# Kernel tuning notes

Hardware: AMD Instinct MI355X
Metric: run time of the kernel (lower is better)

Reference implementation:

```python
import jax, jax.numpy as jnp
import numpy as np

B, S, D_MODEL, NUM_HEADS, DFF = 4, 2048, 256, 8, 1024
DEPTH = D_MODEL // NUM_HEADS
EPS = 1e-6
LENGTH_SCALE = 1.0


def setup_inputs() -> dict:
    key = jax.random.key(0)
    ks = jax.random.split(key, 18)
    n = lambda k, shp, s=0.05: (jax.random.normal(k, shp, dtype=jnp.float32) * s)
    return {
        "x": jax.random.normal(ks[0], (B, S, D_MODEL), dtype=jnp.float32),
        "wq_w": n(ks[1], (D_MODEL, D_MODEL)), "wq_b": jnp.zeros((D_MODEL,), jnp.float32),
        "wk_w": n(ks[2], (D_MODEL, D_MODEL)), "wk_b": jnp.zeros((D_MODEL,), jnp.float32),
        "wv_w": n(ks[3], (D_MODEL, D_MODEL)), "wv_b": jnp.zeros((D_MODEL,), jnp.float32),
        "wo_w": n(ks[4], (D_MODEL, D_MODEL)), "wo_b": jnp.zeros((D_MODEL,), jnp.float32),
        "ffn1_w": n(ks[5], (D_MODEL, DFF)), "ffn1_b": jnp.zeros((DFF,), jnp.float32),
        "ffn2_w": n(ks[6], (DFF, D_MODEL)), "ffn2_b": jnp.zeros((D_MODEL,), jnp.float32),
        "ln1_g": jnp.ones((D_MODEL,), jnp.float32), "ln1_b": jnp.zeros((D_MODEL,), jnp.float32),
        "ln2_g": jnp.ones((D_MODEL,), jnp.float32), "ln2_b": jnp.zeros((D_MODEL,), jnp.float32),
    }


def _layernorm(x, g, b):
    mu = jnp.mean(x, axis=-1, keepdims=True)
    var = jnp.mean(jnp.square(x - mu), axis=-1, keepdims=True)
    return (x - mu) * jax.lax.rsqrt(var + EPS) * g + b


def _split_heads(t):
    # [B,S,D_MODEL] -> [B,H,S,depth]
    return t.reshape(B, S, NUM_HEADS, DEPTH).transpose(0, 2, 1, 3)


def _encoder_layer(x, wq_w, wq_b, wk_w, wk_b, wv_w, wv_b, wo_w, wo_b,
                   ffn1_w, ffn1_b, ffn2_w, ffn2_b, ln1_g, ln1_b, ln2_g, ln2_b):
    q = _split_heads(x @ wq_w + wq_b)
    k = _split_heads(x @ wk_w + wk_b)
    v = _split_heads(x @ wv_w + wv_b)
    # pairwise squared distances: ||q||^2 - 2 q.k + ||k||^2 -> [B,H,S,S]
    q2 = jnp.sum(q * q, axis=-1)  # [B,H,S]
    k2 = jnp.sum(k * k, axis=-1)  # [B,H,S]
    dists = q2[..., :, None] - 2.0 * jnp.einsum("bhqd,bhkd->bhqk", q, k) + k2[..., None, :]
    # exponentiated-quadratic kernel, then softmax over keys (mask=None)
    attn = jax.nn.softmax(jnp.exp(-0.5 * dists / (LENGTH_SCALE ** 2)), axis=-1)
    out = jnp.einsum("bhqk,bhkd->bhqd", attn, v)  # [B,H,S,depth]
    out = out.transpose(0, 2, 1, 3).reshape(B, S, D_MODEL)
    attn_out = out @ wo_w + wo_b
    # dropout is identity (training=False)
    out1 = _layernorm(x + attn_out, ln1_g, ln1_b)
    ffn = jax.nn.relu(out1 @ ffn1_w + ffn1_b) @ ffn2_w + ffn2_b
    return _layernorm(out1 + ffn, ln2_g, ln2_b)


def reference(x, wq_w, wq_b, wk_w, wk_b, wv_w, wv_b, wo_w, wo_b,
              ffn1_w, ffn1_b, ffn2_w, ffn2_b, ln1_g, ln1_b, ln2_g, ln2_b):
    return _encoder_layer(x, wq_w, wq_b, wk_w, wk_b, wv_w, wv_b, wo_w, wo_b,
                          ffn1_w, ffn1_b, ffn2_w, ffn2_b, ln1_g, ln1_b, ln2_g, ln2_b)
```

## Files before the change

kernel.cpp:

```cpp
#include <hip/hip_runtime.h>
#include <hip/hip_bf16.h>

#define SQL  2048
#define DM   256
#define LNEPS 1e-6f
#define NLOG2E_H (-0.72134752f)
#define LOG2E    (1.44269504f)

#define B_XB    (0ull)
#define B_QB    (4ull<<20)
#define B_KB    (8ull<<20)
#define B_VB    (12ull<<20)
#define B_CTX   (16ull<<20)
#define B_O1B   (20ull<<20)
#define B_MID   (24ull<<20)
#define B_WQKVT (40ull<<20)
#define B_WOT   (41ull<<20)
#define B_W1T   (42ull<<20)
#define B_W2T   (43ull<<20)
#define B_BQKV  (44ull<<20)
#define B_HQ    (45ull<<20)
#define B_HK    (46ull<<20)
#define B_C1    (47ull<<20)
#define B_O1F   (55ull<<20)
#define B_C2    (63ull<<20)

typedef float  f32x16 __attribute__((ext_vector_type(16)));
typedef short  bf16x8 __attribute__((ext_vector_type(8)));
typedef int    i32x4  __attribute__((ext_vector_type(4)));
typedef int    i32x2  __attribute__((ext_vector_type(2)));

static __device__ __forceinline__ unsigned short bfu(float f){
    __hip_bfloat16 h = __float2bfloat16(f);
    return *reinterpret_cast<unsigned short*>(&h);
}
static __device__ __forceinline__ unsigned pk2(float a, float b){
    return (unsigned)bfu(a) | ((unsigned)bfu(b) << 16);
}
static __device__ __forceinline__ void glds16(const void* g, void* l){
    __builtin_amdgcn_global_load_lds((const __attribute__((address_space(1))) unsigned int*)g,
                                     (__attribute__((address_space(3))) unsigned int*)l, 16, 0, 0);
}

__global__ __launch_bounds__(256) void k_pack(const float* __restrict__ W,
                                              unsigned short* __restrict__ Wt,
                                              int K, int N)
{
    __shared__ float tile[32][33];
    const int t = threadIdx.x;
    const int tx = t & 31, ty = t >> 5;
    const int kb = blockIdx.x * 32, nb = blockIdx.y * 32;
#pragma unroll
    for (int i = 0; i < 32; i += 8) tile[ty + i][tx] = W[(size_t)(kb + ty + i) * N + nb + tx];
    __syncthreads();
#pragma unroll
    for (int i = 0; i < 32; i += 8) Wt[(size_t)(nb + ty + i) * K + kb + tx] = bfu(tile[tx][ty + i]);
}

__global__ __launch_bounds__(256) void k_packb(const float* __restrict__ bq,
                                               const float* __restrict__ bk,
                                               const float* __restrict__ bv,
                                               float* __restrict__ bqkv)
{
    const int wb = blockIdx.x;
    const float* s = (wb == 0) ? bq : (wb == 1 ? bk : bv);
    bqkv[wb * 256 + threadIdx.x] = s[threadIdx.x];
}

__global__ __launch_bounds__(256) void k_xb(const float* __restrict__ x,
                                            unsigned short* __restrict__ xb)
{
    const int i = blockIdx.x * 256 + threadIdx.x;
    float4 v = ((const float4*)x)[i];
    ushort4 o; o.x = bfu(v.x); o.y = bfu(v.y); o.z = bfu(v.z); o.w = bfu(v.w);
    ((ushort4*)xb)[i] = o;
}

__global__ __launch_bounds__(256, 2) void k_qkv(
    const unsigned short* __restrict__ A, const unsigned short* __restrict__ Bt,
    const float* __restrict__ bias,
    unsigned short* __restrict__ qb, unsigned short* __restrict__ kb,
    unsigned short* __restrict__ vb)
{
    __shared__ __align__(16) char As[16384];
    __shared__ __align__(16) char Bs[16384];
    const int t = threadIdx.x;
    const int lane = t & 63, w = t >> 6;
    const int lo = lane & 31, hi = lane >> 5;
    const int row0 = blockIdx.x * 128;
    const int col0 = blockIdx.y * 128;
    f32x16 acc[2][2] = {};
    const int gS = lane & 7;

    for (int kt = 0; kt < 4; ++kt) {
        const int k0 = kt * 64;
#pragma unroll
        for (int i = 0; i < 4; ++i) {
            const int r = w * 32 + i * 8 + (lane >> 3);
            glds16((const char*)(A  + (size_t)(row0 + r) * 256 + k0) + ((gS ^ (r & 7)) << 4),
                   As + w * 4096 + i * 1024 + lane * 16);
            glds16((const char*)(Bt + (size_t)(col0 + r) * 256 + k0) + ((gS ^ (r & 7)) << 4),
                   Bs + w * 4096 + i * 1024 + lane * 16);
        }
        __syncthreads();
        const int rA = (w >> 1) * 64 + lo;
        const int rB = (w & 1) * 64 + lo;
#pragma unroll
        for (int s = 0; s < 4; ++s) {
            const int g = s * 2 + hi;
            bf16x8 fa0 = *(const bf16x8*)(As + rA * 128 + ((g ^ (rA & 7)) << 4));
            bf16x8 fa1 = *(const bf16x8*)(As + (rA + 32) * 128 + ((g ^ (rA & 7)) << 4));
            bf16x8 fb0 = *(const bf16x8*)(Bs + rB * 128 + ((g ^ (rB & 7)) << 4));
            bf16x8 fb1 = *(const bf16x8*)(Bs + (rB + 32) * 128 + ((g ^ (rB & 7)) << 4));
            acc[0][0] = __builtin_amdgcn_mfma_f32_32x32x16_bf16(fa0, fb0, acc[0][0], 0, 0, 0);
            acc[0][1] = __builtin_amdgcn_mfma_f32_32x32x16_bf16(fa0, fb1, acc[0][1], 0, 0, 0);
            acc[1][0] = __builtin_amdgcn_mfma_f32_32x32x16_bf16(fa1, fb0, acc[1][0], 0, 0, 0);
            acc[1][1] = __builtin_amdgcn_mfma_f32_32x32x16_bf16(fa1, fb1, acc[1][1], 0, 0, 0);
        }
        __syncthreads();
    }
#pragma unroll
    for (int m = 0; m < 2; ++m)
#pragma unroll
    for (int n = 0; n < 2; ++n) {
        const int c0 = col0 + (w & 1) * 64 + n * 32;
        const int which = c0 >> 8, h = (c0 >> 5) & 7;
        unsigned short* dst = (which == 0) ? qb : (which == 1 ? kb : vb);
        const float bv = bias[c0 + lo];
#pragma unroll
        for (int r = 0; r < 16; ++r) {
            const int gr = row0 + (w >> 1) * 64 + m * 32 + (r & 3) + 8 * (r >> 2) + 4 * hi;
            const int b = gr >> 11, s = gr & 2047;
            dst[(((size_t)(b * 8 + h)) * SQL + s) * 32 + lo] = bfu(acc[m][n][r] + bv);
        }
    }
}

__global__ __launch_bounds__(256) void k_h2(const unsigned short* __restrict__ qb,
                                            const unsigned short* __restrict__ kb,
                                            float* __restrict__ hq, float* __restrict__ hk)
{
    const int gid = blockIdx.x * 256 + threadIdx.x;
    const unsigned short* qp = qb + (size_t)gid * 32;
    const unsigned short* kp = kb + (size_t)gid * 32;
    float sq = 0.f, sk = 0.f;
#pragma unroll
    for (int i = 0; i < 4; ++i) {
        i32x4 qv = *(const i32x4*)(qp + i * 8);
        i32x4 kv = *(const i32x4*)(kp + i * 8);
#pragma unroll
        for (int j = 0; j < 4; ++j) {
            unsigned int qw = (unsigned int)qv[j], kw = (unsigned int)kv[j];
            float a = __builtin_bit_cast(float, qw << 16);
            float c = __builtin_bit_cast(float, qw & 0xffff0000u);
            float d = __builtin_bit_cast(float, kw << 16);
            float e = __builtin_bit_cast(float, kw & 0xffff0000u);
            sq += a * a + c * c; sk += d * d + e * e;
        }
    }
    hq[gid] = NLOG2E_H * sq;
    hk[gid] = NLOG2E_H * sk;
}

__global__ __launch_bounds__(256) void k_attn(
    const unsigned short* __restrict__ qg, const unsigned short* __restrict__ kg,
    const unsigned short* __restrict__ vg, const float* __restrict__ hq,
    const float* __restrict__ hk, unsigned short* __restrict__ ctxb)
{
    __shared__ __align__(16) char kls[4096];
    __shared__ __align__(16) char vtl[4096];
    __shared__ __align__(16) float hks[64];
    __shared__ __align__(16) float invs[128];

    const int t = threadIdx.x;
    const int lane = t & 63;
    const int wv_ = t >> 6;
    const int lo = lane & 31;
    const int hi = lane >> 5;

    const int bid = blockIdx.x;
    const int qchunk = bid & 15;
    const int bh = bid >> 4;
    const int b = bh >> 3, h = bh & 7;

    const int qrow = qchunk * 128 + wv_ * 32 + lo;
    const unsigned short* qp = qg + ((size_t)bh * SQL + qrow) * 32;
    bf16x8 qf[2];
    qf[0] = *(const bf16x8*)(qp + hi * 8);
    qf[1] = *(const bf16x8*)(qp + 16 + hi * 8);
    const float hqv = hq[(size_t)bh * SQL + qrow];

    f32x16 acc = {};
    float den = 0.f;

    const int vr_key = t >> 2;
    const int vr_g   = t & 3;
    const unsigned short* kbg = kg + (size_t)bh * SQL * 32;
    const unsigned short* vbg = vg + (size_t)bh * SQL * 32;

    for (int kt = 0; kt < 32; ++kt) {
        const int key0 = kt * 64;
        {
            const int r = (wv_ << 4) + (lane >> 2);
            const int gl = lane & 3;
            glds16((const char*)(kbg + (size_t)(key0 + r) * 32) + ((gl ^ ((r >> 1) & 3)) << 4),
                   kls + wv_ * 1024 + lane * 16);
            const unsigned short* vr = vbg + (size_t)(key0 + vr_key) * 32 + vr_g * 8;
            i32x4 vl = *(const i32x4*)vr;
#pragma unroll
            for (int j2 = 0; j2 < 4; ++j2) {
                unsigned int wrd = (unsigned int)vl[j2];
                const int d0 = vr_g * 8 + j2 * 2;
                *(unsigned short*)(vtl + d0 * 128 + ((vr_key * 2) ^ ((d0 & 7) << 4))) = (unsigned short)(wrd & 0xffff);
                *(unsigned short*)(vtl + (d0 + 1) * 128 + ((vr_key * 2) ^ (((d0 + 1) & 7) << 4))) = (unsigned short)(wrd >> 16);
            }
            if (t < 64) hks[t] = hk[(size_t)bh * SQL + key0 + t];
        }
        __syncthreads();

#pragma unroll
        for (int h2 = 0; h2 < 2; ++h2) {
            const int kb32 = h2 * 32;
            const int kA = kb32 + lo;
            const char* krow = kls + kA * 64;
            const int ksw = (kA >> 1) & 3;
            bf16x8 kf0 = *(const bf16x8*)(krow + (((0 + hi) ^ ksw) << 4));
            bf16x8 kf1 = *(const bf16x8*)(krow + (((2 + hi) ^ ksw) << 4));
            f32x16 sc = {};
            sc = __builtin_amdgcn_mfma_f32_32x32x16_bf16(kf0, qf[0], sc, 0, 0, 0);
            sc = __builtin_amdgcn_mfma_f32_32x32x16_bf16(kf1, qf[1], sc, 0, 0, 0);
            float4 h0 = *(const float4*)&hks[kb32 + 4 * hi];
            float4 h1 = *(const float4*)&hks[kb32 + 8 + 4 * hi];
            float4 h2v = *(const float4*)&hks[kb32 + 16 + 4 * hi];
            float4 h3 = *(const float4*)&hks[kb32 + 24 + 4 * hi];
            float hkv[16] = {h0.x,h0.y,h0.z,h0.w, h1.x,h1.y,h1.z,h1.w,
                             h2v.x,h2v.y,h2v.z,h2v.w, h3.x,h3.y,h3.z,h3.w};
            float w[16];
#pragma unroll
            for (int r = 0; r < 16; ++r) {
                float arg = fmaf(sc[r], LOG2E, hqv + hkv[r]);
                float e1  = __builtin_amdgcn_exp2f(arg);
                float ww  = __builtin_amdgcn_exp2f(e1 * LOG2E);
                den += ww;
                w[r] = ww;
            }
            i32x4 p0; p0[0]=pk2(w[0],w[1]);  p0[1]=pk2(w[2],w[3]);
                      p0[2]=pk2(w[4],w[5]);  p0[3]=pk2(w[6],w[7]);
            i32x4 p1; p1[0]=pk2(w[8],w[9]);  p1[1]=pk2(w[10],w[11]);
                      p1[2]=pk2(w[12],w[13]); p1[3]=pk2(w[14],w[15]);
            const char* vrow = vtl + lo * 128;
            const int vxor = (lo & 7) << 4;
            const int o0 = (kb32 + 4 * hi) * 2;
            const int o1 = (kb32 + 16 + 4 * hi) * 2;
            i32x2 a0 = *(const i32x2*)(vrow + (o0 ^ vxor));
            i32x2 a1 = *(const i32x2*)(vrow + ((o0 + 16) ^ vxor));
            i32x2 b0 = *(const i32x2*)(vrow + (o1 ^ vxor));
            i32x2 b1 = *(const i32x2*)(vrow + ((o1 + 16) ^ vxor));
            i32x4 vb0; vb0[0]=a0[0]; vb0[1]=a0[1]; vb0[2]=a1[0]; vb0[3]=a1[1];
            i32x4 vb1; vb1[0]=b0[0]; vb1[1]=b0[1]; vb1[2]=b1[0]; vb1[3]=b1[1];
            acc = __builtin_amdgcn_mfma_f32_32x32x16_bf16(
                __builtin_bit_cast(bf16x8, p0), __builtin_bit_cast(bf16x8, vb0), acc, 0, 0, 0);
            acc = __builtin_amdgcn_mfma_f32_32x32x16_bf16(
                __builtin_bit_cast(bf16x8, p1), __builtin_bit_cast(bf16x8, vb1), acc, 0, 0, 0);
        }
        __syncthreads();
    }

    const float dfull = den + __shfl_xor(den, 32);
    if (lane < 32) invs[wv_ * 32 + lo] = 1.f / dfull;
    __syncthreads();
    float4 i0 = *(const float4*)&invs[wv_ * 32 + 4 * hi];
    float4 i1 = *(const float4*)&invs[wv_ * 32 + 8 + 4 * hi];
    float4 i2 = *(const float4*)&invs[wv_ * 32 + 16 + 4 * hi];
    float4 i3 = *(const float4*)&invs[wv_ * 32 + 24 + 4 * hi];
    float iv[16] = {i0.x,i0.y,i0.z,i0.w, i1.x,i1.y,i1.z,i1.w,
                    i2.x,i2.y,i2.z,i2.w, i3.x,i3.y,i3.z,i3.w};
    unsigned short* cbase = ctxb + ((size_t)(b * SQL + qchunk * 128 + wv_ * 32)) * 256 + h * 32 + lo;
#pragma unroll
    for (int r = 0; r < 16; ++r) {
        const int qr = (r & 3) + 8 * (r >> 2) + 4 * hi;
        cbase[(size_t)qr * 256] = bfu(acc[r] * iv[r]);
    }
}

template<int KDIM, int NFULL, int RELU, int RESID, int OUTF, int OUTB>
__global__ __launch_bounds__(256, 2) void k_gemm(
    const unsigned short* __restrict__ A, const unsigned short* __restrict__ Bt,
    const float* __restrict__ bias, const float* __restrict__ resid,
    float* __restrict__ outf, unsigned short* __restrict__ outb)
{
    __shared__ __align__(16) char As[16384];
    __shared__ __align__(16) char Bs[16384];
    const int t = threadIdx.x;
    const int lane = t & 63, w = t >> 6;
    const int lo = lane & 31, hi = lane >> 5;
    const int row0 = blockIdx.x * 128;
    const int col0 = blockIdx.y * 128;
    f32x16 acc[2][2] = {};
    const int gS = lane & 7;

    for (int kt = 0; kt < KDIM / 64; ++kt) {
        const int k0 = kt * 64;
#pragma unroll
        for (int i = 0; i < 4; ++i) {
            const int r = w * 32 + i * 8 + (lane >> 3);
            glds16((const char*)(A  + (size_t)(row0 + r) * KDIM + k0) + ((gS ^ (r & 7)) << 4),
                   As + w * 4096 + i * 1024 + lane * 16);
            glds16((const char*)(Bt + (size_t)(col0 + r) * KDIM + k0) + ((gS ^ (r & 7)) << 4),
                   Bs + w * 4096 + i * 1024 + lane * 16);
        }
        __syncthreads();
        const int rA = (w >> 1) * 64 + lo;
        const int rB = (w & 1) * 64 + lo;
#pragma unroll
        for (int s = 0; s < 4; ++s) {
            const int g = s * 2 + hi;
            bf16x8 fa0 = *(const bf16x8*)(As + rA * 128 + ((g ^ (rA & 7)) << 4));
            bf16x8 fa1 = *(const bf16x8*)(As + (rA + 32) * 128 + ((g ^ (rA & 7)) << 4));
            bf16x8 fb0 = *(const bf16x8*)(Bs + rB * 128 + ((g ^ (rB & 7)) << 4));
            bf16x8 fb1 = *(const bf16x8*)(Bs + (rB + 32) * 128 + ((g ^ (rB & 7)) << 4));
            acc[0][0] = __builtin_amdgcn_mfma_f32_32x32x16_bf16(fa0, fb0, acc[0][0], 0, 0, 0);
            acc[0][1] = __builtin_amdgcn_mfma_f32_32x32x16_bf16(fa0, fb1, acc[0][1], 0, 0, 0);
            acc[1][0] = __builtin_amdgcn_mfma_f32_32x32x16_bf16(fa1, fb0, acc[1][0], 0, 0, 0);
            acc[1][1] = __builtin_amdgcn_mfma_f32_32x32x16_bf16(fa1, fb1, acc[1][1], 0, 0, 0);
        }
        __syncthreads();
    }
#pragma unroll
    for (int m = 0; m < 2; ++m)
#pragma unroll
    for (int n = 0; n < 2; ++n) {
        const int c0 = col0 + (w & 1) * 64 + n * 32;
        const float bv = bias[c0 + lo];
#pragma unroll
        for (int r = 0; r < 16; ++r) {
            const int gr = row0 + (w >> 1) * 64 + m * 32 + (r & 3) + 8 * (r >> 2) + 4 * hi;
            float vv = acc[m][n][r] + bv;
            if (RESID) vv += resid[(size_t)gr * NFULL + c0 + lo];
            if (RELU)  vv = fmaxf(vv, 0.f);
            if (OUTF)  outf[(size_t)gr * NFULL + c0 + lo] = vv;
            if (OUTB)  outb[(size_t)gr * NFULL + c0 + lo] = bfu(vv);
        }
    }
}

template<int DUAL>
__global__ __launch_bounds__(256) void k_ln(const float* __restrict__ in,
                                            const float* __restrict__ g,
                                            const float* __restrict__ bt,
                                            float* __restrict__ outf,
                                            unsigned short* __restrict__ outb)
{
    const int row = blockIdx.x * 4 + (threadIdx.x >> 6);
    const int lane = threadIdx.x & 63;
    const float4 v = ((const float4*)(in + (size_t)row * 256))[lane];
    float s  = v.x + v.y + v.z + v.w;
    float ss = v.x * v.x + v.y * v.y + v.z * v.z + v.w * v.w;
#pragma unroll
    for (int off = 32; off; off >>= 1) { s += __shfl_xor(s, off); ss += __shfl_xor(ss, off); }
    const float mu = s * (1.f / 256.f);
    const float rstd = rsqrtf(ss * (1.f / 256.f) - mu * mu + LNEPS);
    const float4 gg = ((const float4*)g)[lane];
    const float4 bb = ((const float4*)bt)[lane];
    float4 o;
    o.x = (v.x - mu) * rstd * gg.x + bb.x;
    o.y = (v.y - mu) * rstd * gg.y + bb.y;
    o.z = (v.z - mu) * rstd * gg.z + bb.z;
    o.w = (v.w - mu) * rstd * gg.w + bb.w;
    ((float4*)(outf + (size_t)row * 256))[lane] = o;
    if (DUAL) {
        ushort4 ob; ob.x = bfu(o.x); ob.y = bfu(o.y); ob.z = bfu(o.z); ob.w = bfu(o.w);
        ((ushort4*)(outb + (size_t)row * 256))[lane] = ob;
    }
}

extern "C" void kernel_launch(void* const* d_in, const int* in_sizes, int n_in,
                              void* d_out, int out_size, void* d_ws, size_t ws_size,
                              hipStream_t stream) {
    const float* x   = (const float*)d_in[0];
    const float* wq  = (const float*)d_in[1];  const float* bq  = (const float*)d_in[2];
    const float* wk  = (const float*)d_in[3];  const float* bk  = (const float*)d_in[4];
    const float* wv  = (const float*)d_in[5];  const float* bv  = (const float*)d_in[6];
    const float* wo  = (const float*)d_in[7];  const float* wob = (const float*)d_in[8];
    const float* w1  = (const float*)d_in[9];  const float* b1  = (const float*)d_in[10];
    const float* w2  = (const float*)d_in[11]; const float* b2  = (const float*)d_in[12];
    const float* g1  = (const float*)d_in[13]; const float* bl1 = (const float*)d_in[14];
    const float* g2  = (const float*)d_in[15]; const float* bl2 = (const float*)d_in[16];

    char* ws = (char*)d_ws;
    unsigned short* xb    = (unsigned short*)(ws + B_XB);
    unsigned short* qb    = (unsigned short*)(ws + B_QB);
    unsigned short* kbuf  = (unsigned short*)(ws + B_KB);
    unsigned short* vbuf  = (unsigned short*)(ws + B_VB);
    unsigned short* ctxb  = (unsigned short*)(ws + B_CTX);
    unsigned short* o1b   = (unsigned short*)(ws + B_O1B);
    unsigned short* mid   = (unsigned short*)(ws + B_MID);
    unsigned short* wqkvT = (unsigned short*)(ws + B_WQKVT);
    unsigned short* woT   = (unsigned short*)(ws + B_WOT);
    unsigned short* w1T   = (unsigned short*)(ws + B_W1T);
    unsigned short* w2T   = (unsigned short*)(ws + B_W2T);
    float* bqkv = (float*)(ws + B_BQKV);
    float* hqb  = (float*)(ws + B_HQ);
    float* hkb  = (float*)(ws + B_HK);
    float* c1   = (float*)(ws + B_C1);
    float* o1f  = (float*)(ws + B_O1F);
    float* c2   = (float*)(ws + B_C2);
    float* out  = (float*)d_out;

    k_pack<<<dim3(8, 8),  dim3(256), 0, stream>>>(wq, wqkvT,             256, 256);
    k_pack<<<dim3(8, 8),  dim3(256), 0, stream>>>(wk, wqkvT + 256 * 256, 256, 256);
    k_pack<<<dim3(8, 8),  dim3(256), 0, stream>>>(wv, wqkvT + 512 * 256, 256, 256);
    k_pack<<<dim3(8, 8),  dim3(256), 0, stream>>>(wo, woT,               256, 256);
    k_pack<<<dim3(8, 32), dim3(256), 0, stream>>>(w1, w1T,               256, 1024);
    k_pack<<<dim3(32, 8), dim3(256), 0, stream>>>(w2, w2T,               1024, 256);
    k_packb<<<dim3(3), dim3(256), 0, stream>>>(bq, bk, bv, bqkv);
    k_xb<<<dim3(2048), dim3(256), 0, stream>>>(x, xb);

    k_qkv<<<dim3(64, 6), dim3(256), 0, stream>>>(xb, wqkvT, bqkv, qb, kbuf, vbuf);
    k_h2<<<dim3(256), dim3(256), 0, stream>>>(qb, kbuf, hqb, hkb);
    k_attn<<<dim3(512), dim3(256), 0, stream>>>(qb, kbuf, vbuf, hqb, hkb, ctxb);
    k_gemm<256, 256, 0, 1, 1, 0><<<dim3(64, 2), dim3(256), 0, stream>>>(ctxb, woT, wob, x, c1, nullptr);
    k_ln<1><<<dim3(2048), dim3(256), 0, stream>>>(c1, g1, bl1, o1f, o1b);

    k_gemm<256, 1024, 1, 0, 0, 1><<<dim3(64, 8), dim3(256), 0, stream>>>(o1b, w1T, b1, nullptr, nullptr, mid);
    k_gemm<1024, 256, 0, 1, 1, 0><<<dim3(64, 2), dim3(256), 0, stream>>>(mid, w2T, b2, o1f, c2, nullptr);
    k_ln<0><<<dim3(2048), dim3(256), 0, stream>>>(c2, g2, bl2, out, nullptr);
}
```

Baseline: 227.6 us.

## Split attention keys across two groups, pre-transpose V, split-K GEMMs, merge pack kernels

Folds the six weight-pack launches, the bias pack and the x conversion into one kernel. The QKV GEMM now writes V pre-transposed and swizzled, so attention can load it straight to LDS with global_load_lds instead of transposing it by hand. Attention runs 512-thread blocks where two groups each take half the keys and reduce through LDS at the end. The Wo and FFN2 GEMMs use split-K into two partial buffers, summed together with the residual inside the layernorm kernel. This raises parallelism and cuts launch count, at the cost of extra partial-sum traffic and an LDS reduction.

```diff
diff --git a/kernel.cpp b/kernel.cpp
--- a/kernel.cpp
+++ b/kernel.cpp
@@ -10,20 +10,19 @@
 #define B_XB    (0ull)
 #define B_QB    (4ull<<20)
 #define B_KB    (8ull<<20)
-#define B_VB    (12ull<<20)
+#define B_VT    (12ull<<20)
 #define B_CTX   (16ull<<20)
 #define B_O1B   (20ull<<20)
-#define B_MID   (24ull<<20)
-#define B_WQKVT (40ull<<20)
-#define B_WOT   (41ull<<20)
-#define B_W1T   (42ull<<20)
-#define B_W2T   (43ull<<20)
-#define B_BQKV  (44ull<<20)
-#define B_HQ    (45ull<<20)
-#define B_HK    (46ull<<20)
-#define B_C1    (47ull<<20)
-#define B_O1F   (55ull<<20)
-#define B_C2    (63ull<<20)
+#define B_O1F   (24ull<<20)
+#define B_MID   (32ull<<20)
+#define B_WQKVT (48ull<<20)
+#define B_WOT   ((48ull<<20)+(512ull<<10))
+#define B_W1T   (49ull<<20)
+#define B_W2T   ((49ull<<20)+(512ull<<10))
+#define B_BQKV  (50ull<<20)
+#define B_HQ    ((50ull<<20)+(64ull<<10))
+#define B_HK    ((50ull<<20)+(320ull<<10))
+#define B_C2    (0ull)
 
 typedef float  f32x16 __attribute__((ext_vector_type(16)));
 typedef short  bf16x8 __attribute__((ext_vector_type(8)));
@@ -42,45 +41,59 @@
                                      (__attribute__((address_space(3))) unsigned int*)l, 16, 0, 0);
 }
 
-__global__ __launch_bounds__(256) void k_pack(const float* __restrict__ W,
-                                              unsigned short* __restrict__ Wt,
-                                              int K, int N)
+__global__ __launch_bounds__(256) void k_packall(
+    const float* __restrict__ wq, const float* __restrict__ wk, const float* __restrict__ wv,
+    const float* __restrict__ wo, const float* __restrict__ w1, const float* __restrict__ w2,
+    const float* __restrict__ bq, const float* __restrict__ bk, const float* __restrict__ bv,
+    const float* __restrict__ x,
+    unsigned short* __restrict__ wqkvT, unsigned short* __restrict__ woT,
+    unsigned short* __restrict__ w1T, unsigned short* __restrict__ w2T,
+    float* __restrict__ bqkv, unsigned short* __restrict__ xb)
 {
     __shared__ float tile[32][33];
+    const int bid = blockIdx.x;
     const int t = threadIdx.x;
-    const int tx = t & 31, ty = t >> 5;
-    const int kb = blockIdx.x * 32, nb = blockIdx.y * 32;
-#pragma unroll
-    for (int i = 0; i < 32; i += 8) tile[ty + i][tx] = W[(size_t)(kb + ty + i) * N + nb + tx];
-    __syncthreads();
-#pragma unroll
-    for (int i = 0; i < 32; i += 8) Wt[(size_t)(nb + ty + i) * K + kb + tx] = bfu(tile[tx][ty + i]);
-}
-
-__global__ __launch_bounds__(256) void k_packb(const float* __restrict__ bq,
-                                               const float* __restrict__ bk,
-                                               const float* __restrict__ bv,
-                                               float* __restrict__ bqkv)
-{
-    const int wb = blockIdx.x;
-    const float* s = (wb == 0) ? bq : (wb == 1 ? bk : bv);
-    bqkv[wb * 256 + threadIdx.x] = s[threadIdx.x];
-}
-
-__global__ __launch_bounds__(256) void k_xb(const float* __restrict__ x,
-                                            unsigned short* __restrict__ xb)
-{
-    const int i = blockIdx.x * 256 + threadIdx.x;
-    float4 v = ((const float4*)x)[i];
-    ushort4 o; o.x = bfu(v.x); o.y = bfu(v.y); o.z = bfu(v.z); o.w = bfu(v.w);
-    ((ushort4*)xb)[i] = o;
+    if (bid < 768) {
+        const float* W; unsigned short* Wt; int K, N, xk, yn;
+        if (bid < 192) {
+            int which = bid >> 6, local = bid & 63;
+            W = (which == 0) ? wq : (which == 1 ? wk : wv);
+            Wt = wqkvT + which * 65536; K = 256; N = 256;
+            xk = local & 7; yn = local >> 3;
+        } else if (bid < 256) {
+            int local = bid - 192; W = wo; Wt = woT; K = 256; N = 256;
+            xk = local & 7; yn = local >> 3;
+        } else if (bid < 512) {
+            int local = bid - 256; W = w1; Wt = w1T; K = 256; N = 1024;
+            xk = local & 7; yn = local >> 3;
+        } else {
+            int local = bid - 512; W = w2; Wt = w2T; K = 1024; N = 256;
+            xk = local & 31; yn = local >> 5;
+        }
+        const int tx = t & 31, ty = t >> 5;
+        const int kb = xk * 32, nb = yn * 32;
+#pragma unroll
+        for (int i = 0; i < 32; i += 8) tile[ty + i][tx] = W[(size_t)(kb + ty + i) * N + nb + tx];
+        __syncthreads();
+#pragma unroll
+        for (int i = 0; i < 32; i += 8) Wt[(size_t)(nb + ty + i) * K + kb + tx] = bfu(tile[tx][ty + i]);
+    } else if (bid < 771) {
+        int wb = bid - 768;
+        const float* s = (wb == 0) ? bq : (wb == 1 ? bk : bv);
+        bqkv[wb * 256 + t] = s[t];
+    } else {
+        const int i = (bid - 771) * 256 + t;
+        float4 v = ((const float4*)x)[i];
+        ushort4 o; o.x = bfu(v.x); o.y = bfu(v.y); o.z = bfu(v.z); o.w = bfu(v.w);
+        ((ushort4*)xb)[i] = o;
+    }
 }
 
 __global__ __launch_bounds__(256, 2) void k_qkv(
     const unsigned short* __restrict__ A, const unsigned short* __restrict__ Bt,
     const float* __restrict__ bias,
     unsigned short* __restrict__ qb, unsigned short* __restrict__ kb,
-    unsigned short* __restrict__ vb)
+    char* __restrict__ vtg)
 {
     __shared__ __align__(16) char As[16384];
     __shared__ __align__(16) char Bs[16384];
@@ -125,13 +138,25 @@
     for (int n = 0; n < 2; ++n) {
         const int c0 = col0 + (w & 1) * 64 + n * 32;
         const int which = c0 >> 8, h = (c0 >> 5) & 7;
-        unsigned short* dst = (which == 0) ? qb : (which == 1 ? kb : vb);
         const float bv = bias[c0 + lo];
-#pragma unroll
-        for (int r = 0; r < 16; ++r) {
-            const int gr = row0 + (w >> 1) * 64 + m * 32 + (r & 3) + 8 * (r >> 2) + 4 * hi;
-            const int b = gr >> 11, s = gr & 2047;
-            dst[(((size_t)(b * 8 + h)) * SQL + s) * 32 + lo] = bfu(acc[m][n][r] + bv);
+        if (which < 2) {
+            unsigned short* dst = (which == 0) ? qb : kb;
+#pragma unroll
+            for (int r = 0; r < 16; ++r) {
+                const int gr = row0 + (w >> 1) * 64 + m * 32 + (r & 3) + 8 * (r >> 2) + 4 * hi;
+                const int b = gr >> 11, s = gr & 2047;
+                dst[(((size_t)(b * 8 + h)) * SQL + s) * 32 + lo] = bfu(acc[m][n][r] + bv);
+            }
+        } else {
+#pragma unroll
+            for (int r = 0; r < 16; ++r) {
+                const int gr = row0 + (w >> 1) * 64 + m * 32 + (r & 3) + 8 * (r >> 2) + 4 * hi;
+                const int b = gr >> 11, s = gr & 2047;
+                const int o = s * 2;
+                const int op = (o & ~0x78) | ((((o >> 3) & 15) ^ (lo & 15)) << 3);
+                *(unsigned short*)(vtg + ((size_t)(b * 8 + h)) * 131072 + (size_t)lo * 4096 + op)
+                    = bfu(acc[m][n][r] + bv);
+            }
         }
     }
 }
@@ -162,26 +187,29 @@
     hk[gid] = NLOG2E_H * sk;
 }
 
-__global__ __launch_bounds__(256) void k_attn(
+__global__ __launch_bounds__(512, 4) void k_attn(
     const unsigned short* __restrict__ qg, const unsigned short* __restrict__ kg,
-    const unsigned short* __restrict__ vg, const float* __restrict__ hq,
+    const char* __restrict__ vtg, const float* __restrict__ hq,
     const float* __restrict__ hk, unsigned short* __restrict__ ctxb)
 {
-    __shared__ __align__(16) char kls[4096];
-    __shared__ __align__(16) char vtl[4096];
-    __shared__ __align__(16) float hks[64];
+    __shared__ __align__(16) char kls[8192];
+    __shared__ __align__(16) char vtl[8192];
+    __shared__ __align__(16) float hks[128];
+    __shared__ __align__(16) float redacc[16 * 256];
+    __shared__ __align__(16) float redden[256];
     __shared__ __align__(16) float invs[128];
 
     const int t = threadIdx.x;
+    const int grp = t >> 8;
+    const int tl = t & 255;
     const int lane = t & 63;
-    const int wv_ = t >> 6;
+    const int wv_ = tl >> 6;
     const int lo = lane & 31;
     const int hi = lane >> 5;
 
     const int bid = blockIdx.x;
     const int qchunk = bid & 15;
     const int bh = bid >> 4;
-    const int b = bh >> 3, h = bh & 7;
 
     const int qrow = qchunk * 128 + wv_ * 32 + lo;
     const unsigned short* qp = qg + ((size_t)bh * SQL + qrow) * 32;
@@ -193,28 +221,20 @@
     f32x16 acc = {};
     float den = 0.f;
 
-    const int vr_key = t >> 2;
-    const int vr_g   = t & 3;
     const unsigned short* kbg = kg + (size_t)bh * SQL * 32;
-    const unsigned short* vbg = vg + (size_t)bh * SQL * 32;
-
-    for (int kt = 0; kt < 32; ++kt) {
-        const int key0 = kt * 64;
+    const char* vtb = vtg + (size_t)bh * 131072;
+    char* kd = kls + grp * 4096;
+    char* vd = vtl + grp * 4096;
+
+    for (int kt = 0; kt < 16; ++kt) {
+        const int key0 = grp * 1024 + kt * 64;
         {
-            const int r = (wv_ << 4) + (lane >> 2);
-            const int gl = lane & 3;
+            const int r = tl >> 2, gl = tl & 3;
             glds16((const char*)(kbg + (size_t)(key0 + r) * 32) + ((gl ^ ((r >> 1) & 3)) << 4),
-                   kls + wv_ * 1024 + lane * 16);
-            const unsigned short* vr = vbg + (size_t)(key0 + vr_key) * 32 + vr_g * 8;
-            i32x4 vl = *(const i32x4*)vr;
-#pragma unroll
-            for (int j2 = 0; j2 < 4; ++j2) {
-                unsigned int wrd = (unsigned int)vl[j2];
-                const int d0 = vr_g * 8 + j2 * 2;
-                *(unsigned short*)(vtl + d0 * 128 + ((vr_key * 2) ^ ((d0 & 7) << 4))) = (unsigned short)(wrd & 0xffff);
-                *(unsigned short*)(vtl + (d0 + 1) * 128 + ((vr_key * 2) ^ (((d0 + 1) & 7) << 4))) = (unsigned short)(wrd >> 16);
-            }
-            if (t < 64) hks[t] = hk[(size_t)bh * SQL + key0 + t];
+                   kd + tl * 16);
+            const int vrw = tl >> 3, vch = tl & 7;
+            glds16(vtb + (size_t)vrw * 4096 + key0 * 2 + vch * 16, vd + tl * 16);
+            if (tl < 64) hks[grp * 64 + tl] = hk[(size_t)bh * SQL + key0 + tl];
         }
         __syncthreads();
 
@@ -222,17 +242,18 @@
         for (int h2 = 0; h2 < 2; ++h2) {
             const int kb32 = h2 * 32;
             const int kA = kb32 + lo;
-            const char* krow = kls + kA * 64;
+            const char* krow = kd + kA * 64;
             const int ksw = (kA >> 1) & 3;
             bf16x8 kf0 = *(const bf16x8*)(krow + (((0 + hi) ^ ksw) << 4));
             bf16x8 kf1 = *(const bf16x8*)(krow + (((2 + hi) ^ ksw) << 4));
             f32x16 sc = {};
             sc = __builtin_amdgcn_mfma_f32_32x32x16_bf16(kf0, qf[0], sc, 0, 0, 0);
             sc = __builtin_amdgcn_mfma_f32_32x32x16_bf16(kf1, qf[1], sc, 0, 0, 0);
-            float4 h0 = *(const float4*)&hks[kb32 + 4 * hi];
-            float4 h1 = *(const float4*)&hks[kb32 + 8 + 4 * hi];
-            float4 h2v = *(const float4*)&hks[kb32 + 16 + 4 * hi];
-            float4 h3 = *(const float4*)&hks[kb32 + 24 + 4 * hi];
+            const float* hb = &hks[grp * 64 + kb32];
+            float4 h0 = *(const float4*)&hb[4 * hi];
+            float4 h1 = *(const float4*)&hb[8 + 4 * hi];
+            float4 h2v = *(const float4*)&hb[16 + 4 * hi];
+            float4 h3 = *(const float4*)&hb[24 + 4 * hi];
             float hkv[16] = {h0.x,h0.y,h0.z,h0.w, h1.x,h1.y,h1.z,h1.w,
                              h2v.x,h2v.y,h2v.z,h2v.w, h3.x,h3.y,h3.z,h3.w};
             float w[16];
@@ -248,8 +269,8 @@
                       p0[2]=pk2(w[4],w[5]);  p0[3]=pk2(w[6],w[7]);
             i32x4 p1; p1[0]=pk2(w[8],w[9]);  p1[1]=pk2(w[10],w[11]);
                       p1[2]=pk2(w[12],w[13]); p1[3]=pk2(w[14],w[15]);
-            const char* vrow = vtl + lo * 128;
-            const int vxor = (lo & 7) << 4;
+            const char* vrow = vd + lo * 128;
+            const int vxor = (lo & 15) << 3;
             const int o0 = (kb32 + 4 * hi) * 2;
             const int o1 = (kb32 + 16 + 4 * hi) * 2;
             i32x2 a0 = *(const i32x2*)(vrow + (o0 ^ vxor));
@@ -266,27 +287,41 @@
         __syncthreads();
     }
 
+    if (grp == 1) {
+#pragma unroll
+        for (int r = 0; r < 16; ++r) redacc[r * 256 + tl] = acc[r];
+        redden[tl] = den;
+    }
+    __syncthreads();
+    if (grp == 0) {
+#pragma unroll
+        for (int r = 0; r < 16; ++r) acc[r] += redacc[r * 256 + tl];
+        den += redden[tl];
+    }
     const float dfull = den + __shfl_xor(den, 32);
-    if (lane < 32) invs[wv_ * 32 + lo] = 1.f / dfull;
+    if (grp == 0 && hi == 0) invs[wv_ * 32 + lo] = 1.f / dfull;
     __syncthreads();
-    float4 i0 = *(const float4*)&invs[wv_ * 32 + 4 * hi];
-    float4 i1 = *(const float4*)&invs[wv_ * 32 + 8 + 4 * hi];
-    float4 i2 = *(const float4*)&invs[wv_ * 32 + 16 + 4 * hi];
-    float4 i3 = *(const float4*)&invs[wv_ * 32 + 24 + 4 * hi];
-    float iv[16] = {i0.x,i0.y,i0.z,i0.w, i1.x,i1.y,i1.z,i1.w,
-                    i2.x,i2.y,i2.z,i2.w, i3.x,i3.y,i3.z,i3.w};
-    unsigned short* cbase = ctxb + ((size_t)(b * SQL + qchunk * 128 + wv_ * 32)) * 256 + h * 32 + lo;
-#pragma unroll
-    for (int r = 0; r < 16; ++r) {
-        const int qr = (r & 3) + 8 * (r >> 2) + 4 * hi;
-        cbase[(size_t)qr * 256] = bfu(acc[r] * iv[r]);
-    }
-}
-
-template<int KDIM, int NFULL, int RELU, int RESID, int OUTF, int OUTB>
+    if (grp == 0) {
+        float4 i0 = *(const float4*)&invs[wv_ * 32 + 4 * hi];
+        float4 i1 = *(const float4*)&invs[wv_ * 32 + 8 + 4 * hi];
+        float4 i2 = *(const float4*)&invs[wv_ * 32 + 16 + 4 * hi];
+        float4 i3 = *(const float4*)&invs[wv_ * 32 + 24 + 4 * hi];
+        float iv[16] = {i0.x,i0.y,i0.z,i0.w, i1.x,i1.y,i1.z,i1.w,
+                        i2.x,i2.y,i2.z,i2.w, i3.x,i3.y,i3.z,i3.w};
+        const int b = bh >> 3, h = bh & 7;
+        unsigned short* cbase = ctxb + ((size_t)(b * SQL + qchunk * 128 + wv_ * 32)) * 256 + h * 32 + lo;
+#pragma unroll
+        for (int r = 0; r < 16; ++r) {
+            const int qr = (r & 3) + 8 * (r >> 2) + 4 * hi;
+            cbase[(size_t)qr * 256] = bfu(acc[r] * iv[r]);
+        }
+    }
+}
+
+template<int KSTRIDE, int KHALF, int NFULL, int RELU, int OUTF, int OUTB>
 __global__ __launch_bounds__(256, 2) void k_gemm(
     const unsigned short* __restrict__ A, const unsigned short* __restrict__ Bt,
-    const float* __restrict__ bias, const float* __restrict__ resid,
+    const float* __restrict__ bias,
     float* __restrict__ outf, unsigned short* __restrict__ outb)
 {
     __shared__ __align__(16) char As[16384];
@@ -296,17 +331,18 @@
     const int lo = lane & 31, hi = lane >> 5;
     const int row0 = blockIdx.x * 128;
     const int col0 = blockIdx.y * 128;
+    const int z = blockIdx.z;
     f32x16 acc[2][2] = {};
     const int gS = lane & 7;
 
-    for (int kt = 0; kt < KDIM / 64; ++kt) {
-        const int k0 = kt * 64;
+    for (int kt = 0; kt < KHALF; ++kt) {
+        const int k0 = (z * KHALF + kt) * 64;
 #pragma unroll
         for (int i = 0; i < 4; ++i) {
             const int r = w * 32 + i * 8 + (lane >> 3);
-            glds16((const char*)(A  + (size_t)(row0 + r) * KDIM + k0) + ((gS ^ (r & 7)) << 4),
+            glds16((const char*)(A  + (size_t)(row0 + r) * KSTRIDE + k0) + ((gS ^ (r & 7)) << 4),
                    As + w * 4096 + i * 1024 + lane * 16);
-            glds16((const char*)(Bt + (size_t)(col0 + r) * KDIM + k0) + ((gS ^ (r & 7)) << 4),
+            glds16((const char*)(Bt + (size_t)(col0 + r) * KSTRIDE + k0) + ((gS ^ (r & 7)) << 4),
                    Bs + w * 4096 + i * 1024 + lane * 16);
         }
         __syncthreads();
@@ -331,29 +367,32 @@
 #pragma unroll
     for (int n = 0; n < 2; ++n) {
         const int c0 = col0 + (w & 1) * 64 + n * 32;
-        const float bv = bias[c0 + lo];
+        const float bv = (z == 0) ? bias[c0 + lo] : 0.f;
 #pragma unroll
         for (int r = 0; r < 16; ++r) {
             const int gr = row0 + (w >> 1) * 64 + m * 32 + (r & 3) + 8 * (r >> 2) + 4 * hi;
             float vv = acc[m][n][r] + bv;
-            if (RESID) vv += resid[(size_t)gr * NFULL + c0 + lo];
-            if (RELU)  vv = fmaxf(vv, 0.f);
-            if (OUTF)  outf[(size_t)gr * NFULL + c0 + lo] = vv;
-            if (OUTB)  outb[(size_t)gr * NFULL + c0 + lo] = bfu(vv);
+            if (RELU) vv = fmaxf(vv, 0.f);
+            if (OUTF) outf[(size_t)z * 8192 * NFULL + (size_t)gr * NFULL + c0 + lo] = vv;
+            if (OUTB) outb[(size_t)gr * NFULL + c0 + lo] = bfu(vv);
         }
     }
 }
 
 template<int DUAL>
-__global__ __launch_bounds__(256) void k_ln(const float* __restrict__ in,
-                                            const float* __restrict__ g,
-                                            const float* __restrict__ bt,
-                                            float* __restrict__ outf,
-                                            unsigned short* __restrict__ outb)
+__global__ __launch_bounds__(256) void k_lnsum(
+    const float* __restrict__ pa, const float* __restrict__ pb,
+    const float* __restrict__ res, const float* __restrict__ g,
+    const float* __restrict__ bt, float* __restrict__ outf,
+    unsigned short* __restrict__ outb)
 {
     const int row = blockIdx.x * 4 + (threadIdx.x >> 6);
     const int lane = threadIdx.x & 63;
-    const float4 v = ((const float4*)(in + (size_t)row * 256))[lane];
+    const size_t base = (size_t)row * 256;
+    float4 v  = ((const float4*)(pa + base))[lane];
+    float4 v2 = ((const float4*)(pb + base))[lane];
+    float4 v3 = ((const float4*)(res + base))[lane];
+    v.x += v2.x + v3.x; v.y += v2.y + v3.y; v.z += v2.z + v3.z; v.w += v2.w + v3.w;
     float s  = v.x + v.y + v.z + v.w;
     float ss = v.x * v.x + v.y * v.y + v.z * v.z + v.w * v.w;
 #pragma unroll
@@ -367,10 +406,10 @@
     o.y = (v.y - mu) * rstd * gg.y + bb.y;
     o.z = (v.z - mu) * rstd * gg.z + bb.z;
     o.w = (v.w - mu) * rstd * gg.w + bb.w;
-    ((float4*)(outf + (size_t)row * 256))[lane] = o;
+    ((float4*)(outf + base))[lane] = o;
     if (DUAL) {
         ushort4 ob; ob.x = bfu(o.x); ob.y = bfu(o.y); ob.z = bfu(o.z); ob.w = bfu(o.w);
-        ((ushort4*)(outb + (size_t)row * 256))[lane] = ob;
+        ((ushort4*)(outb + base))[lane] = ob;
     }
 }
 
@@ -391,10 +430,13 @@
     unsigned short* xb    = (unsigned short*)(ws + B_XB);
     unsigned short* qb    = (unsigned short*)(ws + B_QB);
     unsigned short* kbuf  = (unsigned short*)(ws + B_KB);
-    unsigned short* vbuf  = (unsigned short*)(ws + B_VB);
+    char*           vt    = (char*)(ws + B_VT);
     unsigned short* ctxb  = (unsigned short*)(ws + B_CTX);
     unsigned short* o1b   = (unsigned short*)(ws + B_O1B);
+    float*          o1f   = (float*)(ws + B_O1F);
     unsigned short* mid   = (unsigned short*)(ws + B_MID);
+    float*          c1    = (float*)(ws + B_MID);
+    float*          c2    = (float*)(ws + B_C2);
     unsigned short* wqkvT = (unsigned short*)(ws + B_WQKVT);
     unsigned short* woT   = (unsigned short*)(ws + B_WOT);
     unsigned short* w1T   = (unsigned short*)(ws + B_W1T);
@@ -402,27 +444,16 @@
     float* bqkv = (float*)(ws + B_BQKV);
     float* hqb  = (float*)(ws + B_HQ);
     float* hkb  = (float*)(ws + B_HK);
-    float* c1   = (float*)(ws + B_C1);
-    float* o1f  = (float*)(ws + B_O1F);
-    float* c2   = (float*)(ws + B_C2);
     float* out  = (float*)d_out;
 
-    k_pack<<<dim3(8, 8),  dim3(256), 0, stream>>>(wq, wqkvT,             256, 256);
-    k_pack<<<dim3(8, 8),  dim3(256), 0, stream>>>(wk, wqkvT + 256 * 256, 256, 256);
-    k_pack<<<dim3(8, 8),  dim3(256), 0, stream>>>(wv, wqkvT + 512 * 256, 256, 256);
-    k_pack<<<dim3(8, 8),  dim3(256), 0, stream>>>(wo, woT,               256, 256);
-    k_pack<<<dim3(8, 32), dim3(256), 0, stream>>>(w1, w1T,               256, 1024);
-    k_pack<<<dim3(32, 8), dim3(256), 0, stream>>>(w2, w2T,               1024, 256);
-    k_packb<<<dim3(3), dim3(256), 0, stream>>>(bq, bk, bv, bqkv);
-    k_xb<<<dim3(2048), dim3(256), 0, stream>>>(x, xb);
-
-    k_qkv<<<dim3(64, 6), dim3(256), 0, stream>>>(xb, wqkvT, bqkv, qb, kbuf, vbuf);
+    k_packall<<<dim3(2819), dim3(256), 0, stream>>>(wq, wk, wv, wo, w1, w2, bq, bk, bv, x,
+                                                    wqkvT, woT, w1T, w2T, bqkv, xb);
+    k_qkv<<<dim3(64, 6), dim3(256), 0, stream>>>(xb, wqkvT, bqkv, qb, kbuf, vt);
     k_h2<<<dim3(256), dim3(256), 0, stream>>>(qb, kbuf, hqb, hkb);
-    k_attn<<<dim3(512), dim3(256), 0, stream>>>(qb, kbuf, vbuf, hqb, hkb, ctxb);
-    k_gemm<256, 256, 0, 1, 1, 0><<<dim3(64, 2), dim3(256), 0, stream>>>(ctxb, woT, wob, x, c1, nullptr);
-    k_ln<1><<<dim3(2048), dim3(256), 0, stream>>>(c1, g1, bl1, o1f, o1b);
-
-    k_gemm<256, 1024, 1, 0, 0, 1><<<dim3(64, 8), dim3(256), 0, stream>>>(o1b, w1T, b1, nullptr, nullptr, mid);
-    k_gemm<1024, 256, 0, 1, 1, 0><<<dim3(64, 2), dim3(256), 0, stream>>>(mid, w2T, b2, o1f, c2, nullptr);
-    k_ln<0><<<dim3(2048), dim3(256), 0, stream>>>(c2, g2, bl2, out, nullptr);
-}
+    k_attn<<<dim3(512), dim3(512), 0, stream>>>(qb, kbuf, vt, hqb, hkb, ctxb);
+    k_gemm<256, 2, 256, 0, 1, 0><<<dim3(64, 2, 2), dim3(256), 0, stream>>>(ctxb, woT, wob, c1, nullptr);
+    k_lnsum<1><<<dim3(2048), dim3(256), 0, stream>>>(c1, c1 + 2097152, x, g1, bl1, o1f, o1b);
+    k_gemm<256, 4, 1024, 1, 0, 1><<<dim3(64, 8, 1), dim3(256), 0, stream>>>(o1b, w1T, b1, nullptr, mid);
+    k_gemm<1024, 8, 256, 0, 1, 0><<<dim3(64, 2, 2), dim3(256), 0, stream>>>(mid, w2T, b2, c2, nullptr);
+    k_lnsum<0><<<dim3(2048), dim3(256), 0, stream>>>(c2, c2 + 2097152, o1f, g2, bl2, out, nullptr);
+}
```

New measurement: 199.2 us. -12.5%, faster.
